# Kernel optimization log

Hardware: AMD Instinct MI355X
Metric: run time of the kernel (lower is better)

## Reference

```python
import jax, jax.numpy as jnp
import numpy as np

B, S, H, D, E = 1, 2048, 16, 64, 1024
STRIDE, LCMP = 16, 32          # compression stride / block
LSEL, TOPN = 64, 16            # selection block size / top-k blocks
WIN = 512                      # sliding window
NEG = jnp.float32(-1e9)


def setup_inputs() -> dict:
    key = jax.random.key(0)
    ks = jax.random.split(key, 5)
    q = jax.random.normal(ks[0], (B, S, H, D), jnp.float32)
    k = jax.random.normal(ks[1], (B, S, H, D), jnp.float32)
    v = jax.random.normal(ks[2], (B, S, H, D), jnp.float32)
    x = jax.random.normal(ks[3], (B, S, E), jnp.float32)
    Wg = jax.random.normal(ks[4], (E, 3), jnp.float32) * 0.02
    bg = jnp.zeros((3,), jnp.float32)
    cu_seqlens = jnp.array([0, S], jnp.int32)
    max_seqlen = S
    return {"q": q, "k": k, "v": v, "x": x, "Wg": Wg, "bg": bg,
            "cu_seqlens": cu_seqlens, "max_seqlen": max_seqlen}


def _nsa_forward(q, k, v, x, Wg, bg):
    scale = 1.0 / np.sqrt(D)
    t = jnp.arange(S)
    num_cmp = (S - LCMP) // STRIDE + 1   # 127
    num_sel = S // LSEL                  # 32

    # ---- branch 1: compressed-KV attention (mean-pooled blocks) ----
    starts = jnp.arange(num_cmp) * STRIDE
    widx = starts[:, None] + jnp.arange(LCMP)          # (num_cmp, LCMP)
    Kc = k[:, widx].mean(axis=2)                        # (B, num_cmp, H, D)
    Vc = v[:, widx].mean(axis=2)
    logits_c = jnp.einsum('bshd,bchd->bhsc', q, Kc) * scale
    # query t may attend only to fully-past compressed blocks
    mask_c = (starts + LCMP)[None, :] <= (t[:, None] + 1)   # (S, num_cmp)
    p_c = jax.nn.softmax(jnp.where(mask_c[None, None], logits_c, NEG), axis=-1)
    valid_c = mask_c.any(axis=-1).astype(q.dtype)           # (S,) zero-out empty rows
    p_c = p_c * valid_c[None, None, :, None]
    o_cmp = jnp.einsum('bhsc,bchd->bshd', p_c, Vc)

    # ---- branch 2: top-k selected-block attention ----
    # map compressed-block scores -> selection-block importance (overlap sum)
    sel_s = jnp.arange(num_sel) * LSEL
    overlap = ((starts[:, None] < sel_s[None, :] + LSEL) &
               (starts[:, None] + LCMP > sel_s[None, :])).astype(q.dtype)  # (num_cmp, num_sel)
    p_sel = jnp.einsum('bhsc,cn->bhsn', p_c, overlap)        # (B,H,S,num_sel)
    _, top_idx = jax.lax.top_k(p_sel, TOPN)                  # (B,H,S,TOPN)
    sel_blk = jax.nn.one_hot(top_idx, num_sel).sum(axis=-2) > 0   # (B,H,S,num_sel)
    own_blk = jax.nn.one_hot(t // LSEL, num_sel) > 0              # always include own block
    sel_blk = sel_blk | own_blk[None, None]
    sel_tok = jnp.repeat(sel_blk, LSEL, axis=-1)             # (B,H,S,S) token-level mask

    causal = t[:, None] >= t[None, :]                        # (S,S)
    logits = jnp.einsum('bshd,bthd->bhst', q, k) * scale     # (B,H,S,S), shared by 2 branches
    a_sel = jax.nn.softmax(jnp.where(sel_tok & causal[None, None], logits, NEG), axis=-1)
    o_sel = jnp.einsum('bhst,bthd->bshd', a_sel, v)

    # ---- branch 3: sliding-window attention ----
    win_mask = causal & (t[:, None] - t[None, :] < WIN)
    a_win = jax.nn.softmax(jnp.where(win_mask[None, None], logits, NEG), axis=-1)
    o_win = jnp.einsum('bhst,bthd->bshd', a_win, v)

    # ---- learned gating over the 3 branches ----
    g = jax.nn.sigmoid(x @ Wg + bg)                          # (B,S,3)
    out = (g[..., 0][..., None, None] * o_cmp +
           g[..., 1][..., None, None] * o_sel +
           g[..., 2][..., None, None] * o_win)
    return out                                               # (B,S,H,D)


def reference(q, k, v, x, Wg, bg, cu_seqlens, max_seqlen):
    return _nsa_forward(q, k, v, x, Wg, bg)
```

## Files before the change

### kernel.cpp

```cpp
#include <hip/hip_runtime.h>
#include <hip/hip_bf16.h>
#include <math.h>

#define H_NUM 16
#define D_DIM 64
#define S_LEN 2048
#define E_DIM 1024
#define NC    127
#define TOPN  16
#define SCALE 0.125f
#define FIXM  16.0f

typedef short s16x8 __attribute__((ext_vector_type(8)));
typedef short s16x4 __attribute__((ext_vector_type(4)));
typedef float f32x4 __attribute__((ext_vector_type(4)));
typedef unsigned short ushort_t;

__device__ __forceinline__ unsigned short f2b(float f) {
    __hip_bfloat16 h = __float2bfloat16(f);
    return *reinterpret_cast<unsigned short*>(&h);
}
__device__ __forceinline__ float b2f(unsigned short u) {
    __hip_bfloat16 h = *reinterpret_cast<__hip_bfloat16*>(&u);
    return __bfloat162float(h);
}
__device__ __forceinline__ s16x8 pack8(float4 a, float4 b) {
    s16x8 r;
    r[0] = (short)f2b(a.x); r[1] = (short)f2b(a.y);
    r[2] = (short)f2b(a.z); r[3] = (short)f2b(a.w);
    r[4] = (short)f2b(b.x); r[5] = (short)f2b(b.y);
    r[6] = (short)f2b(b.z); r[7] = (short)f2b(b.w);
    return r;
}
__device__ __forceinline__ f32x4 mfma16(s16x8 a, s16x8 b, f32x4 c) {
    return __builtin_amdgcn_mfma_f32_16x16x32_bf16(a, b, c, 0, 0, 0);
}
__device__ __forceinline__ void wave_lds_fence() {
    asm volatile("s_waitcnt lgkmcnt(0)" ::: "memory");
    __builtin_amdgcn_sched_barrier(0);
}
__device__ __forceinline__ int swP(int r, int c) { return r * 128 + (c ^ ((r & 7) << 2)); }
__device__ __forceinline__ int swU(int r, int c) { return r * 64  + (c ^ ((r & 7) << 3)); }

__device__ __forceinline__ float wave_sum(float v) {
#pragma unroll
    for (int off = 32; off; off >>= 1) v += __shfl_xor(v, off, 64);
    return v;
}

__global__ __launch_bounds__(64) void nsa_compress(
    const float* __restrict__ k, const float* __restrict__ v,
    ushort_t* __restrict__ KcHi, ushort_t* __restrict__ KcLo, ushort_t* __restrict__ VcT)
{
    int bid = blockIdx.x;
    int h = bid >> 7, c = bid & 127;
    int lane = threadIdx.x;
    float mk = 0.f, mv = 0.f;
    if (c < NC) {
        int s0 = c * 16;
#pragma unroll 4
        for (int i = 0; i < 32; ++i) {
            mk += k[((size_t)(s0 + i) * H_NUM + h) * D_DIM + lane];
            mv += v[((size_t)(s0 + i) * H_NUM + h) * D_DIM + lane];
        }
        mk *= (1.f / 32.f); mv *= (1.f / 32.f);
    }
    unsigned short khi = f2b(mk);
    KcHi[((size_t)h * 128 + c) * 64 + lane] = khi;
    KcLo[((size_t)h * 128 + c) * 64 + lane] = f2b(mk - b2f(khi));
    VcT[((size_t)h * 64 + lane) * 128 + c] = f2b(mv);
}

__global__ __launch_bounds__(256) void nsa_cast_k(
    const float* __restrict__ k, ushort_t* __restrict__ Kb)
{
    int idx = (blockIdx.x * 256 + threadIdx.x) * 4;
    int d = idx & 63, s = (idx >> 6) & 2047, h = idx >> 17;
    float4 f = *(const float4*)(k + ((size_t)s * H_NUM + h) * D_DIM + d);
    s16x4 u;
    u[0] = (short)f2b(f.x); u[1] = (short)f2b(f.y);
    u[2] = (short)f2b(f.z); u[3] = (short)f2b(f.w);
    *(s16x4*)(Kb + idx) = u;
}

__global__ __launch_bounds__(256) void nsa_cast_vt(
    const float* __restrict__ v, ushort_t* __restrict__ VtB)
{
    __shared__ ushort_t T[64][136];
    int h = blockIdx.x >> 4, s0 = (blockIdx.x & 15) << 7;
    int tid = threadIdx.x;
#pragma unroll
    for (int rep = 0; rep < 8; ++rep) {
        int idx = rep * 256 + tid;
        int i = idx >> 4, d4 = (idx & 15) << 2;
        float4 f = *(const float4*)(v + ((size_t)(s0 + i) * H_NUM + h) * D_DIM + d4);
        T[d4 + 0][i] = f2b(f.x); T[d4 + 1][i] = f2b(f.y);
        T[d4 + 2][i] = f2b(f.z); T[d4 + 3][i] = f2b(f.w);
    }
    __syncthreads();
    int d = tid >> 2, i0 = (tid & 3) << 5;
    ushort_t* dst = VtB + ((size_t)h * 64 + d) * 2048 + s0 + i0;
#pragma unroll
    for (int jj = 0; jj < 32; jj += 8)
        *(s16x8*)(dst + jj) = *(const s16x8*)&T[d][i0 + jj];
}

__global__ __launch_bounds__(64) void nsa_gate(
    const float* __restrict__ x, const float* __restrict__ Wg,
    const float* __restrict__ bg, float* __restrict__ g)
{
    int s = blockIdx.x, lane = threadIdx.x;
    float a0 = 0.f, a1 = 0.f, a2 = 0.f;
    for (int i = lane; i < E_DIM; i += 64) {
        float xv = x[(size_t)s * E_DIM + i];
        a0 = fmaf(xv, Wg[i * 3 + 0], a0);
        a1 = fmaf(xv, Wg[i * 3 + 1], a1);
        a2 = fmaf(xv, Wg[i * 3 + 2], a2);
    }
    a0 = wave_sum(a0); a1 = wave_sum(a1); a2 = wave_sum(a2);
    if (lane == 0) {
        g[s * 3 + 0] = 1.f / (1.f + expf(-(a0 + bg[0])));
        g[s * 3 + 1] = 1.f / (1.f + expf(-(a1 + bg[1])));
        g[s * 3 + 2] = 1.f / (1.f + expf(-(a2 + bg[2])));
    }
}

__global__ __launch_bounds__(512, 4) void nsa_main(
    const float* __restrict__ q,
    const ushort_t* __restrict__ Kb, const ushort_t* __restrict__ VtB,
    const ushort_t* __restrict__ KcHi, const ushort_t* __restrict__ KcLo,
    const ushort_t* __restrict__ VcT,
    const float* __restrict__ gat, float* __restrict__ out)
{
    __shared__ __align__(16) float    P1[4 * 2048];
    __shared__ __align__(16) float    psl[4 * 512];
    __shared__ __align__(16) ushort_t BP[4 * 2048];
    __shared__ float    mrg[4 * 32];
    __shared__ unsigned selm_l[64];

    const int bid  = blockIdx.x;
    const int h    = bid & 15;
    const int grp  = bid >> 4;
    const int tile = (grp < 16) ? (31 - grp) : (grp - 16);
    const int t0   = tile << 6;
    const int tid  = threadIdx.x;
    const int w    = tid >> 6;
    const int pair = w & 3;
    const bool isA = w < 4;
    const int lane = tid & 63;
    const int lr   = lane & 15;
    const int g    = lane >> 4;
    const int rb   = t0 + 16 * pair;

    float*    P1w  = P1 + pair * 2048;
    float*    pslw = psl + pair * 512;
    ushort_t* APb  = (ushort_t*)pslw;
    ushort_t* BPw  = BP + pair * 2048;
    float*    mrgw = mrg + pair * 32;

    int trow[4];
#pragma unroll
    for (int r = 0; r < 4; ++r) trow[r] = rb + 4 * g + r;

    s16x8 qa[2], ql[2];
    {
        const float* qrow = q + ((size_t)(rb + lr) * H_NUM + h) * D_DIM;
#pragma unroll
        for (int kk = 0; kk < 2; ++kk) {
            float4 a = *(const float4*)(qrow + kk * 32 + g * 8);
            float4 b = *(const float4*)(qrow + kk * 32 + g * 8 + 4);
            s16x8 hi = pack8(a, b);
            float4 ar, br;
            ar.x = a.x - b2f((unsigned short)hi[0]); ar.y = a.y - b2f((unsigned short)hi[1]);
            ar.z = a.z - b2f((unsigned short)hi[2]); ar.w = a.w - b2f((unsigned short)hi[3]);
            br.x = b.x - b2f((unsigned short)hi[4]); br.y = b.y - b2f((unsigned short)hi[5]);
            br.z = b.z - b2f((unsigned short)hi[6]); br.w = b.w - b2f((unsigned short)hi[7]);
            qa[kk] = hi;
            ql[kk] = pack8(ar, br);
        }
    }

    int nv[4];
#pragma unroll
    for (int r = 0; r < 4; ++r) nv[r] = (trow[r] >= 31) ? (((trow[r] - 31) >> 4) + 1) : 0;

    float l1[4] = {0.f, 0.f, 0.f, 0.f};
    f32x4 oc[4];
#pragma unroll
    for (int dt = 0; dt < 4; ++dt) { f32x4 z = {0.f, 0.f, 0.f, 0.f}; oc[dt] = z; }

    const int winlo = (tile >= 8) ? (tile - 8) : 0;
    float l3[4] = {0.f, 0.f, 0.f, 0.f};
    f32x4 o3[4];
#pragma unroll
    for (int dt = 0; dt < 4; ++dt) { f32x4 z = {0.f, 0.f, 0.f, 0.f}; o3[dt] = z; }

    if (isA) {
        f32x4 sc8[8];
#pragma unroll
        for (int ct = 0; ct < 8; ++ct) {
            f32x4 acc = {0.f, 0.f, 0.f, 0.f};
#pragma unroll
            for (int kk = 0; kk < 2; ++kk) {
                const size_t off = ((size_t)h * 128 + 16 * ct + lr) * 64 + kk * 32 + g * 8;
                s16x8 khi = *(const s16x8*)(KcHi + off);
                s16x8 klo = *(const s16x8*)(KcLo + off);
                acc = mfma16(qa[kk], khi, acc);
                acc = mfma16(ql[kk], khi, acc);
                acc = mfma16(qa[kk], klo, acc);
            }
            sc8[ct] = acc;
        }

#pragma unroll
        for (int ct = 0; ct < 8; ++ct)
#pragma unroll
            for (int r = 0; r < 4; ++r) {
                int c = 16 * ct + lr;
                float p = (c < nv[r]) ? __expf(fmaf(sc8[ct][r], SCALE, -FIXM)) : 0.f;
                l1[r] += p;
                P1w[swP(4 * g + r, 16 * ct + lr)] = p;
            }
        wave_lds_fence();

#pragma unroll
        for (int rep = 0; rep < 8; ++rep) {
            int item = rep * 64 + lane;
            int n = item >> 4, row = item & 15;
            int lo = 4 * n - 1; if (lo < 0) lo = 0;
            int hi = 4 * n + 3; if (hi > NC - 1) hi = NC - 1;
            float s = 0.f;
            for (int c = lo; c <= hi; ++c) s += P1w[swP(row, c)];
            pslw[n * 16 + row] = s;
        }
        wave_lds_fence();

        unsigned mymask = 0u;
        {
            float pv[32];
#pragma unroll
            for (int n = 0; n < 32; ++n) pv[n] = (lane < 16) ? pslw[n * 16 + lane] : 0.f;
            for (int it = 0; it < TOPN; ++it) {
                float best = -1.f; int bi = 0;
#pragma unroll
                for (int n = 0; n < 32; ++n) {
                    float val = ((mymask >> n) & 1u) ? -2.f : pv[n];
                    if (val > best) { best = val; bi = n; }
                }
                mymask |= 1u << bi;
            }
        }
        if (lane < 16) selm_l[pair * 16 + lane] = mymask | (1u << tile);

#pragma unroll
        for (int kk = 0; kk < 4; ++kk) {
            float4 a0 = *(const float4*)&P1w[swP(lr, kk * 32 + g * 8)];
            float4 a1 = *(const float4*)&P1w[swP(lr, kk * 32 + g * 8 + 4)];
            s16x8 pa = pack8(a0, a1);
#pragma unroll
            for (int dt = 0; dt < 4; ++dt)
                oc[dt] = mfma16(pa, *(const s16x8*)(VcT + ((size_t)h * 64 + 16 * dt + lr) * 128 + kk * 32 + g * 8), oc[dt]);
        }
#pragma unroll
        for (int off = 8; off >= 1; off >>= 1)
#pragma unroll
            for (int r = 0; r < 4; ++r) l1[r] += __shfl_xor(l1[r], off, 64);
    } else {
        for (int n = winlo; n <= tile; ++n) {
            const int base = n << 6;
            f32x4 s4[4];
#pragma unroll
            for (int ct = 0; ct < 4; ++ct) {
                f32x4 acc = {0.f, 0.f, 0.f, 0.f};
#pragma unroll
                for (int kk = 0; kk < 2; ++kk)
                    acc = mfma16(qa[kk],
                        *(const s16x8*)(Kb + ((size_t)h * 2048 + base + 16 * ct + lr) * 64 + kk * 32 + g * 8), acc);
                s4[ct] = acc;
            }
#pragma unroll
            for (int ct = 0; ct < 4; ++ct)
#pragma unroll
                for (int r = 0; r < 4; ++r) {
                    int j = base + 16 * ct + lr;
                    bool ok = (j >= trow[r] - 511) && (j <= trow[r]);
                    float p = ok ? __expf(fmaf(s4[ct][r], SCALE, -FIXM)) : 0.f;
                    l3[r] += p;
                    BPw[swU(4 * g + r, 16 * ct + lr)] = f2b(p);
                }
            wave_lds_fence();
#pragma unroll
            for (int kk = 0; kk < 2; ++kk) {
                s16x8 pa = *(const s16x8*)&BPw[swU(lr, kk * 32 + g * 8)];
#pragma unroll
                for (int dt = 0; dt < 4; ++dt)
                    o3[dt] = mfma16(pa,
                        *(const s16x8*)(VtB + ((size_t)h * 64 + 16 * dt + lr) * 2048 + base + kk * 32 + g * 8), o3[dt]);
            }
        }
#pragma unroll
        for (int off = 8; off >= 1; off >>= 1)
#pragma unroll
            for (int r = 0; r < 4; ++r) l3[r] += __shfl_xor(l3[r], off, 64);
    }
    __syncthreads();

    unsigned um = selm_l[pair * 16 + lr];
#pragma unroll
    for (int off = 8; off >= 1; off >>= 1) um |= __shfl_xor(um, off, 64);
    unsigned selreg[4];
#pragma unroll
    for (int r = 0; r < 4; ++r) selreg[r] = selm_l[pair * 16 + 4 * g + r];

    float l2[4] = {0.f, 0.f, 0.f, 0.f};
    f32x4 o2[4];
#pragma unroll
    for (int dt = 0; dt < 4; ++dt) { f32x4 z = {0.f, 0.f, 0.f, 0.f}; o2[dt] = z; }

    ushort_t* myP = isA ? APb : (BPw + 1024);
    int cnt = 0;
    for (int n = 0; n <= tile; ++n) {
        if (!((um >> n) & 1u)) continue;
        bool mine = ((cnt & 1) == (isA ? 0 : 1));
        ++cnt;
        if (!mine) continue;
        const int base = n << 6;

        f32x4 s4[4];
#pragma unroll
        for (int ct = 0; ct < 4; ++ct) {
            f32x4 acc = {0.f, 0.f, 0.f, 0.f};
#pragma unroll
            for (int kk = 0; kk < 2; ++kk)
                acc = mfma16(qa[kk],
                    *(const s16x8*)(Kb + ((size_t)h * 2048 + base + 16 * ct + lr) * 64 + kk * 32 + g * 8), acc);
            s4[ct] = acc;
        }
#pragma unroll
        for (int ct = 0; ct < 4; ++ct)
#pragma unroll
            for (int r = 0; r < 4; ++r) {
                int j = base + 16 * ct + lr;
                bool ok = ((selreg[r] >> n) & 1u) && (j <= trow[r]);
                float p = ok ? __expf(fmaf(s4[ct][r], SCALE, -FIXM)) : 0.f;
                l2[r] += p;
                myP[swU(4 * g + r, 16 * ct + lr)] = f2b(p);
            }
        wave_lds_fence();
#pragma unroll
        for (int kk = 0; kk < 2; ++kk) {
            s16x8 pa = *(const s16x8*)&myP[swU(lr, kk * 32 + g * 8)];
#pragma unroll
            for (int dt = 0; dt < 4; ++dt)
                o2[dt] = mfma16(pa,
                    *(const s16x8*)(VtB + ((size_t)h * 64 + 16 * dt + lr) * 2048 + base + kk * 32 + g * 8), o2[dt]);
        }
    }
#pragma unroll
    for (int off = 8; off >= 1; off >>= 1)
#pragma unroll
        for (int r = 0; r < 4; ++r) l2[r] += __shfl_xor(l2[r], off, 64);

    if (!isA) {
#pragma unroll
        for (int dt = 0; dt < 4; ++dt)
#pragma unroll
            for (int r = 0; r < 4; ++r) {
                P1w[(4 * g + r) * 64 + 16 * dt + lr] = o2[dt][r];
                P1w[1024 + (4 * g + r) * 64 + 16 * dt + lr] = o3[dt][r];
            }
        if (lr == 0)
#pragma unroll
            for (int r = 0; r < 4; ++r) {
                mrgw[(4 * g + r) * 2 + 0] = l2[r];
                mrgw[(4 * g + r) * 2 + 1] = l3[r];
            }
    }
    __syncthreads();

    if (isA) {
#pragma unroll
        for (int r = 0; r < 4; ++r) {
            const int row = 4 * g + r;
            float l2f = l2[r] + mrgw[row * 2 + 0];
            float l3B = mrgw[row * 2 + 1];
            const float* gp = gat + (size_t)trow[r] * 3;
            float g0 = gp[0], g1 = gp[1], g2 = gp[2];
            float invc = nv[r] ? (1.f / l1[r]) : 0.f;
            float i2 = 1.f / l2f, i3 = 1.f / l3B;
#pragma unroll
            for (int dt = 0; dt < 4; ++dt) {
                float o2f = o2[dt][r] + P1w[row * 64 + 16 * dt + lr];
                float o3f = P1w[1024 + row * 64 + 16 * dt + lr];
                float val = g0 * (oc[dt][r] * invc) + g1 * (o2f * i2) + g2 * (o3f * i3);
                out[((size_t)trow[r] * H_NUM + h) * D_DIM + 16 * dt + lr] = val;
            }
        }
    }
}

extern "C" void kernel_launch(void* const* d_in, const int* in_sizes, int n_in,
                              void* d_out, int out_size, void* d_ws, size_t ws_size,
                              hipStream_t stream) {
    const float* q  = (const float*)d_in[0];
    const float* k  = (const float*)d_in[1];
    const float* v  = (const float*)d_in[2];
    const float* x  = (const float*)d_in[3];
    const float* Wg = (const float*)d_in[4];
    const float* bg = (const float*)d_in[5];
    float* out = (float*)d_out;

    ushort_t* Kb   = (ushort_t*)d_ws;
    ushort_t* VtB  = Kb  + (size_t)16 * 2048 * 64;
    ushort_t* KcHi = VtB + (size_t)16 * 64 * 2048;
    ushort_t* KcLo = KcHi + (size_t)16 * 128 * 64;
    ushort_t* VcT  = KcLo + (size_t)16 * 128 * 64;
    float*    g    = (float*)(VcT + (size_t)16 * 64 * 128);

    nsa_compress<<<16 * 128, 64, 0, stream>>>(k, v, KcHi, KcLo, VcT);
    nsa_cast_k  <<<2048, 256, 0, stream>>>(k, Kb);
    nsa_cast_vt <<<256, 256, 0, stream>>>(v, VtB);
    nsa_gate    <<<S_LEN, 64, 0, stream>>>(x, Wg, bg, g);
    nsa_main    <<<512, 512, 0, stream>>>(q, Kb, VtB, KcHi, KcLo, VcT, g, out);
}
```

Before: 137.2 us.

## Merge prep kernels into one launch, prefetch V fragments, rebalance selected-block split

```diff
diff --git a/kernel.cpp b/kernel.cpp
--- a/kernel.cpp
+++ b/kernel.cpp
@@ -48,80 +48,82 @@
     return v;
 }
 
-__global__ __launch_bounds__(64) void nsa_compress(
+#define A_SEL_MASK 0x5AD5u
+
+__global__ __launch_bounds__(256) void nsa_prep(
     const float* __restrict__ k, const float* __restrict__ v,
-    ushort_t* __restrict__ KcHi, ushort_t* __restrict__ KcLo, ushort_t* __restrict__ VcT)
+    const float* __restrict__ x, const float* __restrict__ Wg, const float* __restrict__ bg,
+    ushort_t* __restrict__ Kb, ushort_t* __restrict__ VtB,
+    ushort_t* __restrict__ KcHi, ushort_t* __restrict__ KcLo, ushort_t* __restrict__ VcT,
+    float* __restrict__ g)
 {
-    int bid = blockIdx.x;
-    int h = bid >> 7, c = bid & 127;
-    int lane = threadIdx.x;
-    float mk = 0.f, mv = 0.f;
-    if (c < NC) {
-        int s0 = c * 16;
+    const int b   = blockIdx.x;
+    const int tid = threadIdx.x;
+
+    if (b < 512) {
+        int idx0 = (b * 256 + tid) * 16;
+#pragma unroll
+        for (int j = 0; j < 16; j += 4) {
+            int id = idx0 + j;
+            int d = id & 63, s = (id >> 6) & 2047, h = id >> 17;
+            float4 f = *(const float4*)(k + ((size_t)s * H_NUM + h) * D_DIM + d);
+            s16x4 u;
+            u[0] = (short)f2b(f.x); u[1] = (short)f2b(f.y);
+            u[2] = (short)f2b(f.z); u[3] = (short)f2b(f.w);
+            *(s16x4*)(Kb + id) = u;
+        }
+    } else if (b < 768) {
+        __shared__ ushort_t T[64][136];
+        int bb = b - 512;
+        int h = bb >> 4, s0 = (bb & 15) << 7;
+#pragma unroll
+        for (int rep = 0; rep < 8; ++rep) {
+            int idx = rep * 256 + tid;
+            int i = idx >> 4, d4 = (idx & 15) << 2;
+            float4 f = *(const float4*)(v + ((size_t)(s0 + i) * H_NUM + h) * D_DIM + d4);
+            T[d4 + 0][i] = f2b(f.x); T[d4 + 1][i] = f2b(f.y);
+            T[d4 + 2][i] = f2b(f.z); T[d4 + 3][i] = f2b(f.w);
+        }
+        __syncthreads();
+        int d = tid >> 2, i0 = (tid & 3) << 5;
+        ushort_t* dst = VtB + ((size_t)h * 64 + d) * 2048 + s0 + i0;
+#pragma unroll
+        for (int jj = 0; jj < 32; jj += 8)
+            *(s16x8*)(dst + jj) = *(const s16x8*)&T[d][i0 + jj];
+    } else if (b < 1280) {
+        int unit = (b - 768) * 4 + (tid >> 6);
+        int h = unit >> 7, c = unit & 127;
+        int lane = tid & 63;
+        float mk = 0.f, mv = 0.f;
+        if (c < NC) {
+            int s0 = c * 16;
 #pragma unroll 4
-        for (int i = 0; i < 32; ++i) {
-            mk += k[((size_t)(s0 + i) * H_NUM + h) * D_DIM + lane];
-            mv += v[((size_t)(s0 + i) * H_NUM + h) * D_DIM + lane];
-        }
-        mk *= (1.f / 32.f); mv *= (1.f / 32.f);
-    }
-    unsigned short khi = f2b(mk);
-    KcHi[((size_t)h * 128 + c) * 64 + lane] = khi;
-    KcLo[((size_t)h * 128 + c) * 64 + lane] = f2b(mk - b2f(khi));
-    VcT[((size_t)h * 64 + lane) * 128 + c] = f2b(mv);
-}
-
-__global__ __launch_bounds__(256) void nsa_cast_k(
-    const float* __restrict__ k, ushort_t* __restrict__ Kb)
-{
-    int idx = (blockIdx.x * 256 + threadIdx.x) * 4;
-    int d = idx & 63, s = (idx >> 6) & 2047, h = idx >> 17;
-    float4 f = *(const float4*)(k + ((size_t)s * H_NUM + h) * D_DIM + d);
-    s16x4 u;
-    u[0] = (short)f2b(f.x); u[1] = (short)f2b(f.y);
-    u[2] = (short)f2b(f.z); u[3] = (short)f2b(f.w);
-    *(s16x4*)(Kb + idx) = u;
-}
-
-__global__ __launch_bounds__(256) void nsa_cast_vt(
-    const float* __restrict__ v, ushort_t* __restrict__ VtB)
-{
-    __shared__ ushort_t T[64][136];
-    int h = blockIdx.x >> 4, s0 = (blockIdx.x & 15) << 7;
-    int tid = threadIdx.x;
-#pragma unroll
-    for (int rep = 0; rep < 8; ++rep) {
-        int idx = rep * 256 + tid;
-        int i = idx >> 4, d4 = (idx & 15) << 2;
-        float4 f = *(const float4*)(v + ((size_t)(s0 + i) * H_NUM + h) * D_DIM + d4);
-        T[d4 + 0][i] = f2b(f.x); T[d4 + 1][i] = f2b(f.y);
-        T[d4 + 2][i] = f2b(f.z); T[d4 + 3][i] = f2b(f.w);
-    }
-    __syncthreads();
-    int d = tid >> 2, i0 = (tid & 3) << 5;
-    ushort_t* dst = VtB + ((size_t)h * 64 + d) * 2048 + s0 + i0;
-#pragma unroll
-    for (int jj = 0; jj < 32; jj += 8)
-        *(s16x8*)(dst + jj) = *(const s16x8*)&T[d][i0 + jj];
-}
-
-__global__ __launch_bounds__(64) void nsa_gate(
-    const float* __restrict__ x, const float* __restrict__ Wg,
-    const float* __restrict__ bg, float* __restrict__ g)
-{
-    int s = blockIdx.x, lane = threadIdx.x;
-    float a0 = 0.f, a1 = 0.f, a2 = 0.f;
-    for (int i = lane; i < E_DIM; i += 64) {
-        float xv = x[(size_t)s * E_DIM + i];
-        a0 = fmaf(xv, Wg[i * 3 + 0], a0);
-        a1 = fmaf(xv, Wg[i * 3 + 1], a1);
-        a2 = fmaf(xv, Wg[i * 3 + 2], a2);
-    }
-    a0 = wave_sum(a0); a1 = wave_sum(a1); a2 = wave_sum(a2);
-    if (lane == 0) {
-        g[s * 3 + 0] = 1.f / (1.f + expf(-(a0 + bg[0])));
-        g[s * 3 + 1] = 1.f / (1.f + expf(-(a1 + bg[1])));
-        g[s * 3 + 2] = 1.f / (1.f + expf(-(a2 + bg[2])));
+            for (int i = 0; i < 32; ++i) {
+                mk += k[((size_t)(s0 + i) * H_NUM + h) * D_DIM + lane];
+                mv += v[((size_t)(s0 + i) * H_NUM + h) * D_DIM + lane];
+            }
+            mk *= (1.f / 32.f); mv *= (1.f / 32.f);
+        }
+        unsigned short khi = f2b(mk);
+        KcHi[((size_t)h * 128 + c) * 64 + lane] = khi;
+        KcLo[((size_t)h * 128 + c) * 64 + lane] = f2b(mk - b2f(khi));
+        VcT[((size_t)h * 64 + lane) * 128 + c] = f2b(mv);
+    } else {
+        int s = (b - 1280) * 4 + (tid >> 6);
+        int lane = tid & 63;
+        float a0 = 0.f, a1 = 0.f, a2 = 0.f;
+        for (int i = lane; i < E_DIM; i += 64) {
+            float xv = x[(size_t)s * E_DIM + i];
+            a0 = fmaf(xv, Wg[i * 3 + 0], a0);
+            a1 = fmaf(xv, Wg[i * 3 + 1], a1);
+            a2 = fmaf(xv, Wg[i * 3 + 2], a2);
+        }
+        a0 = wave_sum(a0); a1 = wave_sum(a1); a2 = wave_sum(a2);
+        if (lane == 0) {
+            g[s * 3 + 0] = 1.f / (1.f + expf(-(a0 + bg[0])));
+            g[s * 3 + 1] = 1.f / (1.f + expf(-(a1 + bg[1])));
+            g[s * 3 + 2] = 1.f / (1.f + expf(-(a2 + bg[2])));
+        }
     }
 }
 
@@ -158,6 +160,9 @@
     ushort_t* BPw  = BP + pair * 2048;
     float*    mrgw = mrg + pair * 32;
 
+    const ushort_t* KbH  = Kb  + (size_t)h * 2048 * 64;
+    const ushort_t* VtBH = VtB + (size_t)h * 64 * 2048;
+
     int trow[4];
 #pragma unroll
     for (int r = 0; r < 4; ++r) trow[r] = rb + 4 * g + r;
@@ -268,6 +273,12 @@
     } else {
         for (int n = winlo; n <= tile; ++n) {
             const int base = n << 6;
+            s16x8 vf[2][4];
+#pragma unroll
+            for (int kk = 0; kk < 2; ++kk)
+#pragma unroll
+                for (int dt = 0; dt < 4; ++dt)
+                    vf[kk][dt] = *(const s16x8*)(VtBH + (size_t)(16 * dt + lr) * 2048 + base + kk * 32 + g * 8);
             f32x4 s4[4];
 #pragma unroll
             for (int ct = 0; ct < 4; ++ct) {
@@ -275,7 +286,7 @@
 #pragma unroll
                 for (int kk = 0; kk < 2; ++kk)
                     acc = mfma16(qa[kk],
-                        *(const s16x8*)(Kb + ((size_t)h * 2048 + base + 16 * ct + lr) * 64 + kk * 32 + g * 8), acc);
+                        *(const s16x8*)(KbH + (size_t)(base + 16 * ct + lr) * 64 + kk * 32 + g * 8), acc);
                 s4[ct] = acc;
             }
 #pragma unroll
@@ -294,8 +305,7 @@
                 s16x8 pa = *(const s16x8*)&BPw[swU(lr, kk * 32 + g * 8)];
 #pragma unroll
                 for (int dt = 0; dt < 4; ++dt)
-                    o3[dt] = mfma16(pa,
-                        *(const s16x8*)(VtB + ((size_t)h * 64 + 16 * dt + lr) * 2048 + base + kk * 32 + g * 8), o3[dt]);
+                    o3[dt] = mfma16(pa, vf[kk][dt], o3[dt]);
             }
         }
 #pragma unroll
@@ -321,11 +331,17 @@
     int cnt = 0;
     for (int n = 0; n <= tile; ++n) {
         if (!((um >> n) & 1u)) continue;
-        bool mine = ((cnt & 1) == (isA ? 0 : 1));
+        bool aTakes = (A_SEL_MASK >> (cnt & 15)) & 1u;
         ++cnt;
-        if (!mine) continue;
+        if (aTakes != isA) continue;
         const int base = n << 6;
 
+        s16x8 vf[2][4];
+#pragma unroll
+        for (int kk = 0; kk < 2; ++kk)
+#pragma unroll
+            for (int dt = 0; dt < 4; ++dt)
+                vf[kk][dt] = *(const s16x8*)(VtBH + (size_t)(16 * dt + lr) * 2048 + base + kk * 32 + g * 8);
         f32x4 s4[4];
 #pragma unroll
         for (int ct = 0; ct < 4; ++ct) {
@@ -333,7 +349,7 @@
 #pragma unroll
             for (int kk = 0; kk < 2; ++kk)
                 acc = mfma16(qa[kk],
-                    *(const s16x8*)(Kb + ((size_t)h * 2048 + base + 16 * ct + lr) * 64 + kk * 32 + g * 8), acc);
+                    *(const s16x8*)(KbH + (size_t)(base + 16 * ct + lr) * 64 + kk * 32 + g * 8), acc);
             s4[ct] = acc;
         }
 #pragma unroll
@@ -352,8 +368,7 @@
             s16x8 pa = *(const s16x8*)&myP[swU(lr, kk * 32 + g * 8)];
 #pragma unroll
             for (int dt = 0; dt < 4; ++dt)
-                o2[dt] = mfma16(pa,
-                    *(const s16x8*)(VtB + ((size_t)h * 64 + 16 * dt + lr) * 2048 + base + kk * 32 + g * 8), o2[dt]);
+                o2[dt] = mfma16(pa, vf[kk][dt], o2[dt]);
         }
     }
 #pragma unroll
@@ -417,9 +432,6 @@
     ushort_t* VcT  = KcLo + (size_t)16 * 128 * 64;
     float*    g    = (float*)(VcT + (size_t)16 * 64 * 128);
 
-    nsa_compress<<<16 * 128, 64, 0, stream>>>(k, v, KcHi, KcLo, VcT);
-    nsa_cast_k  <<<2048, 256, 0, stream>>>(k, Kb);
-    nsa_cast_vt <<<256, 256, 0, stream>>>(v, VtB);
-    nsa_gate    <<<S_LEN, 64, 0, stream>>>(x, Wg, bg, g);
-    nsa_main    <<<512, 512, 0, stream>>>(q, Kb, VtB, KcHi, KcLo, VcT, g, out);
-}
+    nsa_prep<<<1792, 256, 0, stream>>>(k, v, x, Wg, bg, Kb, VtB, KcHi, KcLo, VcT, g);
+    nsa_main<<<512, 512, 0, stream>>>(q, Kb, VtB, KcHi, KcLo, VcT, g, out);
+}
```

New measurement: 179.8 us. 31.0% more time.
